# Kernel optimization log

Hardware: AMD Instinct MI355X
Metric: run time of the kernel (lower is better)

## Reference

```python
import jax, jax.numpy as jnp
import numpy as np

B, S, DIN, DH, DOUT = 8, 2048, 512, 1024, 16


def setup_inputs() -> dict:
    key = jax.random.key(0)
    ks = jax.random.split(key, 7)
    x = jax.random.normal(ks[0], (B, S, DIN), dtype=jnp.float32)
    # MLP params (Linear stores W as [in, out] here; we apply x @ W + b)
    w1 = jax.random.normal(ks[1], (DIN, DH), dtype=jnp.float32) / np.sqrt(DIN)
    b1 = jnp.zeros((DH,), dtype=jnp.float32)
    w2 = jax.random.normal(ks[2], (DH, DH), dtype=jnp.float32) / np.sqrt(DH)
    b2 = jnp.zeros((DH,), dtype=jnp.float32)
    w3 = jax.random.normal(ks[3], (DH, DOUT), dtype=jnp.float32) / np.sqrt(DH)
    b3 = jnp.zeros((DOUT,), dtype=jnp.float32)
    # decay buffer: exact dyadics 1 - 2^-(c+3), matches init_kwargs list
    decay = 1.0 - 2.0 ** (-(jnp.arange(DOUT, dtype=jnp.float32) + 3.0))
    # D[i, t, c] = decay_c^(t - i) for t >= i else 0 (upper triangular per channel)
    idx = jnp.arange(S)
    exps = idx[None, :] - idx[:, None]            # [S, S], t - i
    mask = (exps >= 0).astype(jnp.float32)        # triu mask
    exps_c = jnp.maximum(exps, 0).astype(jnp.float32)
    D = mask[:, :, None] * (decay[None, None, :] ** exps_c[:, :, None])  # [S, S, DOUT]
    return {"input_temporal": x, "w1": w1, "b1": b1, "w2": w2, "b2": b2,
            "w3": w3, "b3": b3, "D": D}


def reference(input_temporal, w1, b1, w2, b2, w3, b3, D):
    # 3-layer MLP (dropout=0 -> identity in eval)
    h = jax.nn.relu(input_temporal @ w1 + b1)
    h = jax.nn.relu(h @ w2 + b2)
    o = h @ w3 + b3                               # [B, S, DOUT]
    # decay-weighted causal mixing: out[b,t,c] = sum_{i<=t} o[b,i,c] * decay_c^(t-i)
    # (equivalent to torch repeat+multiply+sum, without materializing [B,S,S,D])
    mixed = jnp.einsum('bic,itc->btc', o, D)
    # extra running cumsum as in the original forward
    return jnp.cumsum(mixed, axis=1)
```

## Files before the change

kernel.cpp:

```cpp
#include <hip/hip_runtime.h>

typedef unsigned int u32;
typedef unsigned short u16;
typedef float f32x4 __attribute__((ext_vector_type(4)));
typedef short bf16x8 __attribute__((ext_vector_type(8)));

__device__ __forceinline__ u16 f2bf(float f) {
  u32 u = __builtin_bit_cast(u32, f);
  u += 0x7FFFu + ((u >> 16) & 1u);
  return (u16)(u >> 16);
}
__device__ __forceinline__ void gload_lds16(const void* g, void* l) {
  __builtin_amdgcn_global_load_lds(
      (const __attribute__((address_space(1))) void*)g,
      (__attribute__((address_space(3))) void*)l, 16, 0, 0);
}

__global__ __launch_bounds__(256) void cast_f32_bf16_k(
    const float4* __restrict__ in, uint2* __restrict__ out, int n4) {
  int i = blockIdx.x * 256 + threadIdx.x;
  if (i < n4) {
    float4 v = in[i];
    uint2 o;
    o.x = (u32)f2bf(v.x) | ((u32)f2bf(v.y) << 16);
    o.y = (u32)f2bf(v.z) | ((u32)f2bf(v.w) << 16);
    out[i] = o;
  }
}

__global__ __launch_bounds__(256) void transpose3_k(
    const float* __restrict__ w1, u16* __restrict__ w1t,
    const float* __restrict__ w2, u16* __restrict__ w2t,
    const float* __restrict__ w3, u16* __restrict__ w3t) {
  __shared__ float tile[32][33];
  const float* in; u16* out; int R, C;
  if (blockIdx.z == 0)      { in = w1; out = w1t; R = 512;  C = 1024; }
  else if (blockIdx.z == 1) { in = w2; out = w2t; R = 1024; C = 1024; }
  else                      { in = w3; out = w3t; R = 1024; C = 16;   }
  int c0 = blockIdx.x * 32, r0 = blockIdx.y * 32;
  if (c0 >= C || r0 >= R) return;
  int tx = threadIdx.x, ty = threadIdx.y;
  #pragma unroll
  for (int j = 0; j < 4; j++) {
    int r = r0 + ty + j * 8, c = c0 + tx;
    if (r < R && c < C) tile[ty + j * 8][tx] = in[(size_t)r * C + c];
  }
  __syncthreads();
  #pragma unroll
  for (int j = 0; j < 4; j++) {
    int c = c0 + ty + j * 8, r = r0 + tx;
    if (r < R && c < C) out[(size_t)c * R + r] = f2bf(tile[tx][ty + j * 8]);
  }
}

__global__ __launch_bounds__(512, 2) void gemm_bt_k(
    const u16* __restrict__ A, const u16* __restrict__ Bt,
    const float* __restrict__ bias, u16* __restrict__ C,
    int M, int N, int K) {
  __shared__ __align__(16) char lds[3 * 49152];
  const int tid = threadIdx.x;
  const int rr = blockIdx.x;
  const int xcd = rr & 7, slot_id = rr >> 3;
  const int bm = (xcd << 3) | (slot_id >> 3);
  const int bn = slot_id & 7;
  const int wave = tid >> 6, lane = tid & 63;
  const int wm = wave >> 1, wn = wave & 1;
  const int l15 = lane & 15, l4 = lane >> 4;
  const int NT = K >> 6;
  const size_t arow0 = (size_t)bm * 256, brow0 = (size_t)bn * 128;

  f32x4 acc[4][4];
  #pragma unroll
  for (int m = 0; m < 4; m++)
    #pragma unroll
    for (int n = 0; n < 4; n++) acc[m][n] = (f32x4){0.f, 0.f, 0.f, 0.f};

  auto stage = [&](int kt, int s) {
    char* sA = lds + s * 49152;
    char* sB = sA + 32768;
    #pragma unroll
    for (int j = 0; j < 4; j++) {
      int ch = tid + j * 512;
      int row = ch >> 3;
      int col8 = (ch & 7) ^ (row & 7);
      gload_lds16(A + (arow0 + row) * K + kt * 64 + col8 * 8, sA + ch * 16);
    }
    #pragma unroll
    for (int j = 0; j < 2; j++) {
      int ch = tid + j * 512;
      int row = ch >> 3;
      int col8 = (ch & 7) ^ (row & 7);
      gload_lds16(Bt + (brow0 + row) * K + kt * 64 + col8 * 8, sB + ch * 16);
    }
  };

  stage(0, 0);
  stage(1, 1);
  asm volatile("s_waitcnt vmcnt(6)" ::: "memory");
  __builtin_amdgcn_s_barrier();

  for (int t = 0; t < NT; t++) {
    const int s = t % 3;
    const char* sA = lds + s * 49152;
    const char* sB = sA + 32768;

    bf16x8 bfr[2][4];
    #pragma unroll
    for (int ks = 0; ks < 2; ks++)
      #pragma unroll
      for (int n = 0; n < 4; n++) {
        int r = wn * 64 + n * 16 + l15;
        bfr[ks][n] = *(const bf16x8*)(sB + r * 128 +
                                      (((ks * 4 + l4) ^ (r & 7)) << 4));
      }
    bf16x8 af0[2][2];
    #pragma unroll
    for (int m = 0; m < 2; m++)
      #pragma unroll
      for (int ks = 0; ks < 2; ks++) {
        int r = wm * 64 + m * 16 + l15;
        af0[m][ks] = *(const bf16x8*)(sA + r * 128 +
                                      (((ks * 4 + l4) ^ (r & 7)) << 4));
      }
    if (t + 2 < NT) stage(t + 2, (t + 2) % 3);

    __builtin_amdgcn_s_barrier();
    asm volatile("s_waitcnt lgkmcnt(0)" ::: "memory");
    __builtin_amdgcn_sched_barrier(0);
    __builtin_amdgcn_s_setprio(1);
    #pragma unroll
    for (int m = 0; m < 2; m++)
      #pragma unroll
      for (int n = 0; n < 4; n++)
        #pragma unroll
        for (int ks = 0; ks < 2; ks++)
          acc[m][n] = __builtin_amdgcn_mfma_f32_16x16x32_bf16(
              af0[m][ks], bfr[ks][n], acc[m][n], 0, 0, 0);
    __builtin_amdgcn_s_setprio(0);

    bf16x8 af1[2][2];
    #pragma unroll
    for (int m = 0; m < 2; m++)
      #pragma unroll
      for (int ks = 0; ks < 2; ks++) {
        int r = wm * 64 + (m + 2) * 16 + l15;
        af1[m][ks] = *(const bf16x8*)(sA + r * 128 +
                                      (((ks * 4 + l4) ^ (r & 7)) << 4));
      }
    __builtin_amdgcn_s_barrier();
    asm volatile("s_waitcnt lgkmcnt(0)" ::: "memory");
    __builtin_amdgcn_sched_barrier(0);
    __builtin_amdgcn_s_setprio(1);
    #pragma unroll
    for (int m = 0; m < 2; m++)
      #pragma unroll
      for (int n = 0; n < 4; n++)
        #pragma unroll
        for (int ks = 0; ks < 2; ks++)
          acc[m + 2][n] = __builtin_amdgcn_mfma_f32_16x16x32_bf16(
              af1[m][ks], bfr[ks][n], acc[m + 2][n], 0, 0, 0);
    __builtin_amdgcn_s_setprio(0);

    if (t + 1 < NT) {
      if (t + 2 < NT)
        asm volatile("s_waitcnt vmcnt(6)" ::: "memory");
      else
        asm volatile("s_waitcnt vmcnt(0)" ::: "memory");
      __builtin_amdgcn_s_barrier();
    }
  }

  #pragma unroll
  for (int n = 0; n < 4; n++) {
    int col = bn * 128 + wn * 64 + n * 16 + l15;
    float bv = bias[col];
    #pragma unroll
    for (int m = 0; m < 4; m++) {
      int row0 = bm * 256 + wm * 64 + m * 16 + l4 * 4;
      #pragma unroll
      for (int r = 0; r < 4; r++) {
        float v = acc[m][n][r] + bv;
        v = v > 0.f ? v : 0.f;
        C[(size_t)(row0 + r) * N + col] = f2bf(v);
      }
    }
  }
}

__global__ __launch_bounds__(512, 2) void gemm2f_k(
    const u16* __restrict__ A, const u16* __restrict__ Bt,
    const float* __restrict__ bias, const u16* __restrict__ w3t,
    float* __restrict__ part, int M, int N, int K) {
  __shared__ __align__(16) char lds[131072];
  const int tid = threadIdx.x;
  const int rr = blockIdx.x;
  const int xcd = rr & 7, slot_id = rr >> 3;
  const int bm = (xcd << 3) | (slot_id >> 2);
  const int bn = slot_id & 3;
  const int wave = tid >> 6, lane = tid & 63;
  const int wm = wave >> 2, wn = wave & 3;
  const int l15 = lane & 15, l4 = lane >> 4;
  const int NT = K >> 5;
  const size_t arow0 = (size_t)bm * 256, brow0 = (size_t)bn * 256;

  f32x4 acc[4][8];
  #pragma unroll
  for (int p = 0; p < 4; p++)
    #pragma unroll
    for (int q = 0; q < 8; q++) acc[p][q] = (f32x4){0.f, 0.f, 0.f, 0.f};

  auto stage = [&](int kt, int s) {
    char* sA = lds + s * 32768;
    char* sB = sA + 16384;
    #pragma unroll
    for (int j = 0; j < 2; j++) {
      int ch = tid + j * 512;
      int row = ch >> 2;
      int col4 = (ch & 3) ^ (row & 3);
      gload_lds16(A + (arow0 + row) * K + kt * 32 + col4 * 8, sA + ch * 16);
    }
    #pragma unroll
    for (int j = 0; j < 2; j++) {
      int ch = tid + j * 512;
      int row = ch >> 2;
      int col4 = (ch & 3) ^ (row & 3);
      gload_lds16(Bt + (brow0 + row) * K + kt * 32 + col4 * 8, sB + ch * 16);
    }
  };

  stage(0, 0);
  stage(1, 1);
  asm volatile("s_waitcnt vmcnt(4)" ::: "memory");
  __builtin_amdgcn_s_barrier();

  for (int t = 0; t < NT; t++) {
    const int s = t % 3;
    const char* sA = lds + s * 32768;
    const char* sB = sA + 16384;

    bf16x8 bfr[4];
    #pragma unroll
    for (int n = 0; n < 4; n++) {
      int r = wn * 64 + n * 16 + l15;
      bfr[n] = *(const bf16x8*)(sB + r * 64 + ((l4 ^ (r & 3)) << 4));
    }
    bf16x8 af0[4];
    #pragma unroll
    for (int m = 0; m < 4; m++) {
      int r = wm * 128 + m * 16 + l15;
      af0[m] = *(const bf16x8*)(sA + r * 64 + ((l4 ^ (r & 3)) << 4));
    }
    if (t + 2 < NT) stage(t + 2, (t + 2) % 3);

    __builtin_amdgcn_s_barrier();
    asm volatile("s_waitcnt lgkmcnt(0)" ::: "memory");
    __builtin_amdgcn_sched_barrier(0);
    __builtin_amdgcn_s_setprio(1);
    #pragma unroll
    for (int p = 0; p < 4; p++)
      #pragma unroll
      for (int q = 0; q < 4; q++)
        acc[p][q] = __builtin_amdgcn_mfma_f32_16x16x32_bf16(
            bfr[p], af0[q], acc[p][q], 0, 0, 0);
    __builtin_amdgcn_s_setprio(0);

    bf16x8 af1[4];
    #pragma unroll
    for (int m = 0; m < 4; m++) {
      int r = wm * 128 + (m + 4) * 16 + l15;
      af1[m] = *(const bf16x8*)(sA + r * 64 + ((l4 ^ (r & 3)) << 4));
    }
    __builtin_amdgcn_s_barrier();
    asm volatile("s_waitcnt lgkmcnt(0)" ::: "memory");
    __builtin_amdgcn_sched_barrier(0);
    __builtin_amdgcn_s_setprio(1);
    #pragma unroll
    for (int p = 0; p < 4; p++)
      #pragma unroll
      for (int q = 0; q < 4; q++)
        acc[p][q + 4] = __builtin_amdgcn_mfma_f32_16x16x32_bf16(
            bfr[p], af1[q], acc[p][q + 4], 0, 0, 0);
    __builtin_amdgcn_s_setprio(0);

    if (t + 1 < NT) {
      if (t + 2 < NT)
        asm volatile("s_waitcnt vmcnt(4)" ::: "memory");
      else
        asm volatile("s_waitcnt vmcnt(0)" ::: "memory");
      __builtin_amdgcn_s_barrier();
    }
  }

  __builtin_amdgcn_s_barrier();
  #pragma unroll
  for (int p = 0; p < 4; p++) {
    float4 bv = *(const float4*)(bias + wn * 64 + p * 16 + l4 * 4);
    int colb = (wn * 64 + p * 16 + l4 * 4) * 2;
    #pragma unroll
    for (int q = 0; q < 8; q++) {
      int hrow = wm * 128 + q * 16 + l15;
      float v0 = acc[p][q][0] + bv.x; v0 = v0 > 0.f ? v0 : 0.f;
      float v1 = acc[p][q][1] + bv.y; v1 = v1 > 0.f ? v1 : 0.f;
      float v2 = acc[p][q][2] + bv.z; v2 = v2 > 0.f ? v2 : 0.f;
      float v3 = acc[p][q][3] + bv.w; v3 = v3 > 0.f ? v3 : 0.f;
      uint2 pk;
      pk.x = (u32)f2bf(v0) | ((u32)f2bf(v1) << 16);
      pk.y = (u32)f2bf(v2) | ((u32)f2bf(v3) << 16);
      *(uint2*)(lds + hrow * 512 + (colb ^ ((hrow & 7) << 4))) = pk;
    }
  }
  __builtin_amdgcn_s_barrier();

  bf16x8 wf[8];
  {
    const u16* w3row = w3t + (size_t)l15 * 1024 + bn * 256 + l4 * 8;
    #pragma unroll
    for (int kk = 0; kk < 8; kk++)
      wf[kk] = *(const bf16x8*)(w3row + kk * 32);
  }
  #pragma unroll
  for (int g = 0; g < 2; g++) {
    int row0 = wave * 32 + g * 16;
    int row = row0 + l15;
    f32x4 oacc = (f32x4){0.f, 0.f, 0.f, 0.f};
    #pragma unroll
    for (int kk = 0; kk < 8; kk++) {
      bf16x8 hf = *(const bf16x8*)(lds + row * 512 +
                                   ((kk * 64 + l4 * 16) ^ ((row & 7) << 4)));
      oacc = __builtin_amdgcn_mfma_f32_16x16x32_bf16(hf, wf[kk], oacc,
                                                     0, 0, 0);
    }
    int grow = bm * 256 + row0 + l4 * 4;
    int b = grow >> 11, s = grow & 2047;
    float4 st = {oacc[0], oacc[1], oacc[2], oacc[3]};
    *(float4*)(part + ((size_t)bn * 128 + b * 16 + l15) * 2048 + s) = st;
  }
}

__global__ __launch_bounds__(64) void scan_k(
    const float* __restrict__ part, const float* __restrict__ b3,
    float* __restrict__ out) {
  const int chain = blockIdx.x;
  const int lane = threadIdx.x;
  const int b = chain >> 4, c = chain & 15;
  const float dinv = __builtin_bit_cast(float, (u32)((127 - (c + 3)) << 23));
  const float d = 1.f - dinv;
  const float b3c = b3[c];

  float o[32];
  #pragma unroll
  for (int i = 0; i < 8; i++) {
    float4 acc4 = {b3c, b3c, b3c, b3c};
    #pragma unroll
    for (int p = 0; p < 4; p++) {
      const float4* src = (const float4*)(part + (size_t)p * 262144 +
                                          (size_t)chain * 2048 + lane * 32);
      float4 v = src[i];
      acc4.x += v.x; acc4.y += v.y; acc4.z += v.z; acc4.w += v.w;
    }
    o[i * 4 + 0] = acc4.x; o[i * 4 + 1] = acc4.y;
    o[i * 4 + 2] = acc4.z; o[i * 4 + 3] = acc4.w;
  }

  float M = 0.f, A = 0.f, P = 1.f, S = 0.f;
  #pragma unroll
  for (int i = 0; i < 32; i++) {
    M = d * M + o[i];
    A += M;
    P *= d;
    S = d * S + d;
  }

  #pragma unroll
  for (int off = 1; off < 64; off <<= 1) {
    float Pp = __shfl_up(P, off, 64);
    float Mp = __shfl_up(M, off, 64);
    float Sp = __shfl_up(S, off, 64);
    float Ap = __shfl_up(A, off, 64);
    if (lane >= off) {
      float A2 = Ap + S * Mp + A;
      float S2 = Sp + S * Pp;
      float M2 = P * Mp + M;
      float P2 = Pp * P;
      A = A2; S = S2; M = M2; P = P2;
    }
  }
  float m0 = __shfl_up(M, 1, 64);
  float a0 = __shfl_up(A, 1, 64);
  if (lane == 0) { m0 = 0.f; a0 = 0.f; }

  float* dst = out + (size_t)b * 32768 + (size_t)(lane * 32) * 16 + c;
  float m = m0, a = a0;
  #pragma unroll
  for (int i = 0; i < 32; i++) {
    m = d * m + o[i];
    a += m;
    dst[i * 16] = a;
  }
}

extern "C" void kernel_launch(void* const* d_in, const int* in_sizes, int n_in,
                              void* d_out, int out_size, void* d_ws, size_t ws_size,
                              hipStream_t stream) {
  const float* x  = (const float*)d_in[0];
  const float* w1 = (const float*)d_in[1];
  const float* b1 = (const float*)d_in[2];
  const float* w2 = (const float*)d_in[3];
  const float* b2 = (const float*)d_in[4];
  const float* w3 = (const float*)d_in[5];
  const float* b3 = (const float*)d_in[6];
  float* out = (float*)d_out;

  char* ws = (char*)d_ws;
  size_t off = 0;
  u16* A1   = (u16*)(ws + off); off += (size_t)16384 * 512 * 2;
  u16* h1   = (u16*)(ws + off); off += (size_t)16384 * 1024 * 2;
  u16* w1t  = (u16*)(ws + off); off += (size_t)1024 * 512 * 2;
  u16* w2t  = (u16*)(ws + off); off += (size_t)1024 * 1024 * 2;
  u16* w3t  = (u16*)(ws + off); off += (size_t)16 * 1024 * 2;
  float* part = (float*)(ws + off); off += (size_t)4 * 128 * 2048 * 4;

  cast_f32_bf16_k<<<8192, 256, 0, stream>>>((const float4*)x, (uint2*)A1,
                                            16384 * 512 / 4);
  transpose3_k<<<dim3(32, 32, 3), dim3(32, 8), 0, stream>>>(
      w1, w1t, w2, w2t, w3, w3t);

  gemm_bt_k<<<512, 512, 0, stream>>>(A1, w1t, b1, h1, 16384, 1024, 512);
  gemm2f_k<<<256, 512, 0, stream>>>(h1, w2t, b2, w3t, part,
                                    16384, 1024, 1024);
  scan_k<<<128, 64, 0, stream>>>(part, b3, out);
}
```

Measured before the change: 85.97 us.

## Fuse fp32-to-bf16 input cast into first GEMM via LDS conversion

Removes the separate cast kernel and the bf16 copy of the input. The first GEMM now stages fp32 input tiles straight into LDS with a K tile of 32, converts them to bf16 with v_cvt_pk_bf16_f32 while loading fragments, and swaps the MFMA operand order so the epilogue can write packed 4-wide bf16 stores with a vector bias load. This saves one full read and write pass over the input and one launch. In exchange it doubles the number of K iterations and barriers per tile, and each A tile now moves twice the bytes into LDS.

```diff
diff --git a/kernel.cpp b/kernel.cpp
--- a/kernel.cpp
+++ b/kernel.cpp
@@ -15,17 +15,10 @@
       (const __attribute__((address_space(1))) void*)g,
       (__attribute__((address_space(3))) void*)l, 16, 0, 0);
 }
-
-__global__ __launch_bounds__(256) void cast_f32_bf16_k(
-    const float4* __restrict__ in, uint2* __restrict__ out, int n4) {
-  int i = blockIdx.x * 256 + threadIdx.x;
-  if (i < n4) {
-    float4 v = in[i];
-    uint2 o;
-    o.x = (u32)f2bf(v.x) | ((u32)f2bf(v.y) << 16);
-    o.y = (u32)f2bf(v.z) | ((u32)f2bf(v.w) << 16);
-    out[i] = o;
-  }
+__device__ __forceinline__ u32 cvtpk_bf16(float lo, float hi) {
+  u32 r;
+  asm("v_cvt_pk_bf16_f32 %0, %1, %2" : "=v"(r) : "v"(lo), "v"(hi));
+  return r;
 }
 
 __global__ __launch_bounds__(256) void transpose3_k(
@@ -53,11 +46,11 @@
   }
 }
 
-__global__ __launch_bounds__(512, 2) void gemm_bt_k(
-    const u16* __restrict__ A, const u16* __restrict__ Bt,
+__global__ __launch_bounds__(512, 2) void gemm1f_k(
+    const float* __restrict__ X, const u16* __restrict__ Bt,
     const float* __restrict__ bias, u16* __restrict__ C,
     int M, int N, int K) {
-  __shared__ __align__(16) char lds[3 * 49152];
+  __shared__ __align__(16) char lds[3 * 40960];
   const int tid = threadIdx.x;
   const int rr = blockIdx.x;
   const int xcd = rr & 7, slot_id = rr >> 3;
@@ -66,62 +59,64 @@
   const int wave = tid >> 6, lane = tid & 63;
   const int wm = wave >> 1, wn = wave & 1;
   const int l15 = lane & 15, l4 = lane >> 4;
-  const int NT = K >> 6;
+  const int NT = K >> 5;
   const size_t arow0 = (size_t)bm * 256, brow0 = (size_t)bn * 128;
 
   f32x4 acc[4][4];
   #pragma unroll
-  for (int m = 0; m < 4; m++)
-    #pragma unroll
-    for (int n = 0; n < 4; n++) acc[m][n] = (f32x4){0.f, 0.f, 0.f, 0.f};
+  for (int n = 0; n < 4; n++)
+    #pragma unroll
+    for (int m = 0; m < 4; m++) acc[n][m] = (f32x4){0.f, 0.f, 0.f, 0.f};
 
   auto stage = [&](int kt, int s) {
-    char* sA = lds + s * 49152;
+    char* sA = lds + s * 40960;
     char* sB = sA + 32768;
     #pragma unroll
     for (int j = 0; j < 4; j++) {
       int ch = tid + j * 512;
       int row = ch >> 3;
-      int col8 = (ch & 7) ^ (row & 7);
-      gload_lds16(A + (arow0 + row) * K + kt * 64 + col8 * 8, sA + ch * 16);
-    }
-    #pragma unroll
-    for (int j = 0; j < 2; j++) {
-      int ch = tid + j * 512;
-      int row = ch >> 3;
-      int col8 = (ch & 7) ^ (row & 7);
-      gload_lds16(Bt + (brow0 + row) * K + kt * 64 + col8 * 8, sB + ch * 16);
+      int g = (ch & 7) ^ (row & 7);
+      gload_lds16(X + (arow0 + row) * K + kt * 32 + g * 4, sA + ch * 16);
+    }
+    {
+      int ch = tid;
+      int row = ch >> 2;
+      int col4 = (ch & 3) ^ (row & 3);
+      gload_lds16(Bt + (brow0 + row) * K + kt * 32 + col4 * 8, sB + ch * 16);
     }
   };
 
   stage(0, 0);
   stage(1, 1);
-  asm volatile("s_waitcnt vmcnt(6)" ::: "memory");
+  asm volatile("s_waitcnt vmcnt(5)" ::: "memory");
   __builtin_amdgcn_s_barrier();
 
   for (int t = 0; t < NT; t++) {
     const int s = t % 3;
-    const char* sA = lds + s * 49152;
+    const char* sA = lds + s * 40960;
     const char* sB = sA + 32768;
 
-    bf16x8 bfr[2][4];
-    #pragma unroll
-    for (int ks = 0; ks < 2; ks++)
-      #pragma unroll
-      for (int n = 0; n < 4; n++) {
-        int r = wn * 64 + n * 16 + l15;
-        bfr[ks][n] = *(const bf16x8*)(sB + r * 128 +
-                                      (((ks * 4 + l4) ^ (r & 7)) << 4));
-      }
-    bf16x8 af0[2][2];
-    #pragma unroll
-    for (int m = 0; m < 2; m++)
-      #pragma unroll
-      for (int ks = 0; ks < 2; ks++) {
-        int r = wm * 64 + m * 16 + l15;
-        af0[m][ks] = *(const bf16x8*)(sA + r * 128 +
-                                      (((ks * 4 + l4) ^ (r & 7)) << 4));
-      }
+    bf16x8 bfr[4];
+    #pragma unroll
+    for (int n = 0; n < 4; n++) {
+      int r = wn * 64 + n * 16 + l15;
+      bfr[n] = *(const bf16x8*)(sB + r * 64 + ((l4 ^ (r & 3)) << 4));
+    }
+    bf16x8 af[4];
+    #pragma unroll
+    for (int m = 0; m < 4; m++) {
+      int r = wm * 64 + m * 16 + l15;
+      int g0 = ((l4 * 2 + 0) ^ (r & 7)) << 4;
+      int g1 = ((l4 * 2 + 1) ^ (r & 7)) << 4;
+      f32x4 a0 = *(const f32x4*)(sA + r * 128 + g0);
+      f32x4 a1 = *(const f32x4*)(sA + r * 128 + g1);
+      u32 p0 = cvtpk_bf16(a0[0], a0[1]);
+      u32 p1 = cvtpk_bf16(a0[2], a0[3]);
+      u32 p2 = cvtpk_bf16(a1[0], a1[1]);
+      u32 p3 = cvtpk_bf16(a1[2], a1[3]);
+      uint4 packed = {p0, p1, p2, p3};
+      af[m] = __builtin_bit_cast(bf16x8, packed);
+    }
     if (t + 2 < NT) stage(t + 2, (t + 2) % 3);
 
     __builtin_amdgcn_s_barrier();
@@ -129,41 +124,16 @@
     __builtin_amdgcn_sched_barrier(0);
     __builtin_amdgcn_s_setprio(1);
     #pragma unroll
-    for (int m = 0; m < 2; m++)
+    for (int n = 0; n < 4; n++)
       #pragma unroll
-      for (int n = 0; n < 4; n++)
-        #pragma unroll
-        for (int ks = 0; ks < 2; ks++)
-          acc[m][n] = __builtin_amdgcn_mfma_f32_16x16x32_bf16(
-              af0[m][ks], bfr[ks][n], acc[m][n], 0, 0, 0);
-    __builtin_amdgcn_s_setprio(0);
-
-    bf16x8 af1[2][2];
-    #pragma unroll
-    for (int m = 0; m < 2; m++)
-      #pragma unroll
-      for (int ks = 0; ks < 2; ks++) {
-        int r = wm * 64 + (m + 2) * 16 + l15;
-        af1[m][ks] = *(const bf16x8*)(sA + r * 128 +
-                                      (((ks * 4 + l4) ^ (r & 7)) << 4));
-      }
-    __builtin_amdgcn_s_barrier();
-    asm volatile("s_waitcnt lgkmcnt(0)" ::: "memory");
-    __builtin_amdgcn_sched_barrier(0);
-    __builtin_amdgcn_s_setprio(1);
-    #pragma unroll
-    for (int m = 0; m < 2; m++)
-      #pragma unroll
-      for (int n = 0; n < 4; n++)
-        #pragma unroll
-        for (int ks = 0; ks < 2; ks++)
-          acc[m + 2][n] = __builtin_amdgcn_mfma_f32_16x16x32_bf16(
-              af1[m][ks], bfr[ks][n], acc[m + 2][n], 0, 0, 0);
+      for (int m = 0; m < 4; m++)
+        acc[n][m] = __builtin_amdgcn_mfma_f32_16x16x32_bf16(
+            bfr[n], af[m], acc[n][m], 0, 0, 0);
     __builtin_amdgcn_s_setprio(0);
 
     if (t + 1 < NT) {
       if (t + 2 < NT)
-        asm volatile("s_waitcnt vmcnt(6)" ::: "memory");
+        asm volatile("s_waitcnt vmcnt(5)" ::: "memory");
       else
         asm volatile("s_waitcnt vmcnt(0)" ::: "memory");
       __builtin_amdgcn_s_barrier();
@@ -172,17 +142,19 @@
 
   #pragma unroll
   for (int n = 0; n < 4; n++) {
-    int col = bn * 128 + wn * 64 + n * 16 + l15;
-    float bv = bias[col];
+    int col0 = bn * 128 + wn * 64 + n * 16 + l4 * 4;
+    float4 bv = *(const float4*)(bias + col0);
     #pragma unroll
     for (int m = 0; m < 4; m++) {
-      int row0 = bm * 256 + wm * 64 + m * 16 + l4 * 4;
-      #pragma unroll
-      for (int r = 0; r < 4; r++) {
-        float v = acc[m][n][r] + bv;
-        v = v > 0.f ? v : 0.f;
-        C[(size_t)(row0 + r) * N + col] = f2bf(v);
-      }
+      int row = bm * 256 + wm * 64 + m * 16 + l15;
+      float v0 = acc[n][m][0] + bv.x; v0 = v0 > 0.f ? v0 : 0.f;
+      float v1 = acc[n][m][1] + bv.y; v1 = v1 > 0.f ? v1 : 0.f;
+      float v2 = acc[n][m][2] + bv.z; v2 = v2 > 0.f ? v2 : 0.f;
+      float v3 = acc[n][m][3] + bv.w; v3 = v3 > 0.f ? v3 : 0.f;
+      uint2 pk;
+      pk.x = (u32)f2bf(v0) | ((u32)f2bf(v1) << 16);
+      pk.y = (u32)f2bf(v2) | ((u32)f2bf(v3) << 16);
+      *(uint2*)(C + (size_t)row * N + col0) = pk;
     }
   }
 }
@@ -413,19 +385,16 @@
 
   char* ws = (char*)d_ws;
   size_t off = 0;
-  u16* A1   = (u16*)(ws + off); off += (size_t)16384 * 512 * 2;
   u16* h1   = (u16*)(ws + off); off += (size_t)16384 * 1024 * 2;
   u16* w1t  = (u16*)(ws + off); off += (size_t)1024 * 512 * 2;
   u16* w2t  = (u16*)(ws + off); off += (size_t)1024 * 1024 * 2;
   u16* w3t  = (u16*)(ws + off); off += (size_t)16 * 1024 * 2;
   float* part = (float*)(ws + off); off += (size_t)4 * 128 * 2048 * 4;
 
-  cast_f32_bf16_k<<<8192, 256, 0, stream>>>((const float4*)x, (uint2*)A1,
-                                            16384 * 512 / 4);
   transpose3_k<<<dim3(32, 32, 3), dim3(32, 8), 0, stream>>>(
       w1, w1t, w2, w2t, w3, w3t);
 
-  gemm_bt_k<<<512, 512, 0, stream>>>(A1, w1t, b1, h1, 16384, 1024, 512);
+  gemm1f_k<<<512, 512, 0, stream>>>(x, w1t, b1, h1, 16384, 1024, 512);
   gemm2f_k<<<256, 512, 0, stream>>>(h1, w2t, b2, w3t, part,
                                     16384, 1024, 1024);
   scan_k<<<128, 64, 0, stream>>>(part, b3, out);
```

After: 93.16 us. 1.08x slower.

## Merge cast and transpose launches; make GEMM1 blocks compute two N tiles

Applied to the files above, without the earlier changes.

The input cast and weight transpose kernels are merged into one launch, with the block index split between the transpose work and the cast work. The first GEMM now launches 256 blocks, and each block loops over two adjacent 128-wide N tiles with the same A rows. The aim is to cut one kernel launch and have one persistent wave of blocks instead of two, improving A reuse through cache. The cost is less parallelism per launch and a serial two-pass loop per block, with A re-staged from global memory on each pass.

```diff
diff --git a/kernel.cpp b/kernel.cpp
--- a/kernel.cpp
+++ b/kernel.cpp
@@ -16,30 +16,32 @@
       (__attribute__((address_space(3))) void*)l, 16, 0, 0);
 }
 
-__global__ __launch_bounds__(256) void cast_f32_bf16_k(
-    const float4* __restrict__ in, uint2* __restrict__ out, int n4) {
-  int i = blockIdx.x * 256 + threadIdx.x;
-  if (i < n4) {
-    float4 v = in[i];
+__global__ __launch_bounds__(256) void prep_k(
+    const float* __restrict__ x, uint2* __restrict__ A1,
+    const float* __restrict__ w1, u16* __restrict__ w1t,
+    const float* __restrict__ w2, u16* __restrict__ w2t,
+    const float* __restrict__ w3, u16* __restrict__ w3t) {
+  const int bid = blockIdx.x;
+  const int tid = threadIdx.x;
+  if (bid >= 3072) {
+    int i = (bid - 3072) * 256 + tid;
+    float4 v = ((const float4*)x)[i];
     uint2 o;
     o.x = (u32)f2bf(v.x) | ((u32)f2bf(v.y) << 16);
     o.y = (u32)f2bf(v.z) | ((u32)f2bf(v.w) << 16);
-    out[i] = o;
-  }
-}
-
-__global__ __launch_bounds__(256) void transpose3_k(
-    const float* __restrict__ w1, u16* __restrict__ w1t,
-    const float* __restrict__ w2, u16* __restrict__ w2t,
-    const float* __restrict__ w3, u16* __restrict__ w3t) {
+    A1[i] = o;
+    return;
+  }
   __shared__ float tile[32][33];
+  const int z = bid >> 10, t = bid & 1023;
+  const int bx = t & 31, by = t >> 5;
   const float* in; u16* out; int R, C;
-  if (blockIdx.z == 0)      { in = w1; out = w1t; R = 512;  C = 1024; }
-  else if (blockIdx.z == 1) { in = w2; out = w2t; R = 1024; C = 1024; }
-  else                      { in = w3; out = w3t; R = 1024; C = 16;   }
-  int c0 = blockIdx.x * 32, r0 = blockIdx.y * 32;
+  if (z == 0)      { in = w1; out = w1t; R = 512;  C = 1024; }
+  else if (z == 1) { in = w2; out = w2t; R = 1024; C = 1024; }
+  else             { in = w3; out = w3t; R = 1024; C = 16;   }
+  int c0 = bx * 32, r0 = by * 32;
   if (c0 >= C || r0 >= R) return;
-  int tx = threadIdx.x, ty = threadIdx.y;
+  int tx = tid & 31, ty = tid >> 5;
   #pragma unroll
   for (int j = 0; j < 4; j++) {
     int r = r0 + ty + j * 8, c = c0 + tx;
@@ -53,135 +55,142 @@
   }
 }
 
-__global__ __launch_bounds__(512, 2) void gemm_bt_k(
+__global__ __launch_bounds__(512, 2) void gemm1p_k(
     const u16* __restrict__ A, const u16* __restrict__ Bt,
     const float* __restrict__ bias, u16* __restrict__ C,
     int M, int N, int K) {
   __shared__ __align__(16) char lds[3 * 49152];
   const int tid = threadIdx.x;
   const int rr = blockIdx.x;
-  const int xcd = rr & 7, slot_id = rr >> 3;
-  const int bm = (xcd << 3) | (slot_id >> 3);
-  const int bn = slot_id & 7;
+  const int xcd = rr & 7, s_id = rr >> 3;
+  const int bm = (xcd << 3) | (s_id >> 2);
+  const int bnBase = (s_id & 3) << 1;
   const int wave = tid >> 6, lane = tid & 63;
   const int wm = wave >> 1, wn = wave & 1;
   const int l15 = lane & 15, l4 = lane >> 4;
   const int NT = K >> 6;
-  const size_t arow0 = (size_t)bm * 256, brow0 = (size_t)bn * 128;
-
-  f32x4 acc[4][4];
-  #pragma unroll
-  for (int m = 0; m < 4; m++)
-    #pragma unroll
-    for (int n = 0; n < 4; n++) acc[m][n] = (f32x4){0.f, 0.f, 0.f, 0.f};
-
-  auto stage = [&](int kt, int s) {
-    char* sA = lds + s * 49152;
-    char* sB = sA + 32768;
-    #pragma unroll
-    for (int j = 0; j < 4; j++) {
-      int ch = tid + j * 512;
-      int row = ch >> 3;
-      int col8 = (ch & 7) ^ (row & 7);
-      gload_lds16(A + (arow0 + row) * K + kt * 64 + col8 * 8, sA + ch * 16);
-    }
-    #pragma unroll
-    for (int j = 0; j < 2; j++) {
-      int ch = tid + j * 512;
-      int row = ch >> 3;
-      int col8 = (ch & 7) ^ (row & 7);
-      gload_lds16(Bt + (brow0 + row) * K + kt * 64 + col8 * 8, sB + ch * 16);
-    }
-  };
-
-  stage(0, 0);
-  stage(1, 1);
-  asm volatile("s_waitcnt vmcnt(6)" ::: "memory");
-  __builtin_amdgcn_s_barrier();
-
-  for (int t = 0; t < NT; t++) {
-    const int s = t % 3;
-    const char* sA = lds + s * 49152;
-    const char* sB = sA + 32768;
-
-    bf16x8 bfr[2][4];
-    #pragma unroll
-    for (int ks = 0; ks < 2; ks++)
-      #pragma unroll
-      for (int n = 0; n < 4; n++) {
-        int r = wn * 64 + n * 16 + l15;
-        bfr[ks][n] = *(const bf16x8*)(sB + r * 128 +
-                                      (((ks * 4 + l4) ^ (r & 7)) << 4));
+  const size_t arow0 = (size_t)bm * 256;
+
+  for (int p = 0; p < 2; p++) {
+    const int bn = bnBase + p;
+    const size_t brow0 = (size_t)bn * 128;
+
+    f32x4 acc[4][4];
+    #pragma unroll
+    for (int m = 0; m < 4; m++)
+      #pragma unroll
+      for (int n = 0; n < 4; n++) acc[m][n] = (f32x4){0.f, 0.f, 0.f, 0.f};
+
+    auto stage = [&](int kt, int s) {
+      char* sA = lds + s * 49152;
+      char* sB = sA + 32768;
+      #pragma unroll
+      for (int j = 0; j < 4; j++) {
+        int ch = tid + j * 512;
+        int row = ch >> 3;
+        int col8 = (ch & 7) ^ (row & 7);
+        gload_lds16(A + (arow0 + row) * K + kt * 64 + col8 * 8, sA + ch * 16);
       }
-    bf16x8 af0[2][2];
-    #pragma unroll
-    for (int m = 0; m < 2; m++)
-      #pragma unroll
-      for (int ks = 0; ks < 2; ks++) {
-        int r = wm * 64 + m * 16 + l15;
-        af0[m][ks] = *(const bf16x8*)(sA + r * 128 +
-                                      (((ks * 4 + l4) ^ (r & 7)) << 4));
+      #pragma unroll
+      for (int j = 0; j < 2; j++) {
+        int ch = tid + j * 512;
+        int row = ch >> 3;
+        int col8 = (ch & 7) ^ (row & 7);
+        gload_lds16(Bt + (brow0 + row) * K + kt * 64 + col8 * 8, sB + ch * 16);
       }
-    if (t + 2 < NT) stage(t + 2, (t + 2) % 3);
-
+    };
+
+    if (p) __builtin_amdgcn_s_barrier();
+
+    stage(0, 0);
+    stage(1, 1);
+    asm volatile("s_waitcnt vmcnt(6)" ::: "memory");
     __builtin_amdgcn_s_barrier();
-    asm volatile("s_waitcnt lgkmcnt(0)" ::: "memory");
-    __builtin_amdgcn_sched_barrier(0);
-    __builtin_amdgcn_s_setprio(1);
-    #pragma unroll
-    for (int m = 0; m < 2; m++)
-      #pragma unroll
-      for (int n = 0; n < 4; n++)
-        #pragma unroll
-        for (int ks = 0; ks < 2; ks++)
-          acc[m][n] = __builtin_amdgcn_mfma_f32_16x16x32_bf16(
-              af0[m][ks], bfr[ks][n], acc[m][n], 0, 0, 0);
-    __builtin_amdgcn_s_setprio(0);
-
-    bf16x8 af1[2][2];
-    #pragma unroll
-    for (int m = 0; m < 2; m++)
-      #pragma unroll
-      for (int ks = 0; ks < 2; ks++) {
-        int r = wm * 64 + (m + 2) * 16 + l15;
-        af1[m][ks] = *(const bf16x8*)(sA + r * 128 +
-                                      (((ks * 4 + l4) ^ (r & 7)) << 4));
+
+    for (int t = 0; t < NT; t++) {
+      const int s = t % 3;
+      const char* sA = lds + s * 49152;
+      const char* sB = sA + 32768;
+
+      bf16x8 bfr[2][4];
+      #pragma unroll
+      for (int ks = 0; ks < 2; ks++)
+        #pragma unroll
+        for (int n = 0; n < 4; n++) {
+          int r = wn * 64 + n * 16 + l15;
+          bfr[ks][n] = *(const bf16x8*)(sB + r * 128 +
+                                        (((ks * 4 + l4) ^ (r & 7)) << 4));
+        }
+      bf16x8 af0[2][2];
+      #pragma unroll
+      for (int m = 0; m < 2; m++)
+        #pragma unroll
+        for (int ks = 0; ks < 2; ks++) {
+          int r = wm * 64 + m * 16 + l15;
+          af0[m][ks] = *(const bf16x8*)(sA + r * 128 +
+                                        (((ks * 4 + l4) ^ (r & 7)) << 4));
+        }
+      if (t + 2 < NT) stage(t + 2, (t + 2) % 3);
+
+      __builtin_amdgcn_s_barrier();
+      asm volatile("s_waitcnt lgkmcnt(0)" ::: "memory");
+      __builtin_amdgcn_sched_barrier(0);
+      __builtin_amdgcn_s_setprio(1);
+      #pragma unroll
+      for (int m = 0; m < 2; m++)
+        #pragma unroll
+        for (int n = 0; n < 4; n++)
+          #pragma unroll
+          for (int ks = 0; ks < 2; ks++)
+            acc[m][n] = __builtin_amdgcn_mfma_f32_16x16x32_bf16(
+                af0[m][ks], bfr[ks][n], acc[m][n], 0, 0, 0);
+      __builtin_amdgcn_s_setprio(0);
+
+      bf16x8 af1[2][2];
+      #pragma unroll
+      for (int m = 0; m < 2; m++)
+        #pragma unroll
+        for (int ks = 0; ks < 2; ks++) {
+          int r = wm * 64 + (m + 2) * 16 + l15;
+          af1[m][ks] = *(const bf16x8*)(sA + r * 128 +
+                                        (((ks * 4 + l4) ^ (r & 7)) << 4));
+        }
+      __builtin_amdgcn_s_barrier();
+      asm volatile("s_waitcnt lgkmcnt(0)" ::: "memory");
+      __builtin_amdgcn_sched_barrier(0);
+      __builtin_amdgcn_s_setprio(1);
+      #pragma unroll
+      for (int m = 0; m < 2; m++)
+        #pragma unroll
+        for (int n = 0; n < 4; n++)
+          #pragma unroll
+          for (int ks = 0; ks < 2; ks++)
+            acc[m + 2][n] = __builtin_amdgcn_mfma_f32_16x16x32_bf16(
+                af1[m][ks], bfr[ks][n], acc[m + 2][n], 0, 0, 0);
+      __builtin_amdgcn_s_setprio(0);
+
+      if (t + 1 < NT) {
+        if (t + 2 < NT)
+          asm volatile("s_waitcnt vmcnt(6)" ::: "memory");
+        else
+          asm volatile("s_waitcnt vmcnt(0)" ::: "memory");
+        __builtin_amdgcn_s_barrier();
       }
-    __builtin_amdgcn_s_barrier();
-    asm volatile("s_waitcnt lgkmcnt(0)" ::: "memory");
-    __builtin_amdgcn_sched_barrier(0);
-    __builtin_amdgcn_s_setprio(1);
-    #pragma unroll
-    for (int m = 0; m < 2; m++)
-      #pragma unroll
-      for (int n = 0; n < 4; n++)
-        #pragma unroll
-        for (int ks = 0; ks < 2; ks++)
-          acc[m + 2][n] = __builtin_amdgcn_mfma_f32_16x16x32_bf16(
-              af1[m][ks], bfr[ks][n], acc[m + 2][n], 0, 0, 0);
-    __builtin_amdgcn_s_setprio(0);
-
-    if (t + 1 < NT) {
-      if (t + 2 < NT)
-        asm volatile("s_waitcnt vmcnt(6)" ::: "memory");
-      else
-        asm volatile("s_waitcnt vmcnt(0)" ::: "memory");
-      __builtin_amdgcn_s_barrier();
-    }
-  }
-
-  #pragma unroll
-  for (int n = 0; n < 4; n++) {
-    int col = bn * 128 + wn * 64 + n * 16 + l15;
-    float bv = bias[col];
-    #pragma unroll
-    for (int m = 0; m < 4; m++) {
-      int row0 = bm * 256 + wm * 64 + m * 16 + l4 * 4;
-      #pragma unroll
-      for (int r = 0; r < 4; r++) {
-        float v = acc[m][n][r] + bv;
-        v = v > 0.f ? v : 0.f;
-        C[(size_t)(row0 + r) * N + col] = f2bf(v);
+    }
+
+    #pragma unroll
+    for (int n = 0; n < 4; n++) {
+      int col = bn * 128 + wn * 64 + n * 16 + l15;
+      float bv = bias[col];
+      #pragma unroll
+      for (int m = 0; m < 4; m++) {
+        int row0 = bm * 256 + wm * 64 + m * 16 + l4 * 4;
+        #pragma unroll
+        for (int r = 0; r < 4; r++) {
+          float v = acc[m][n][r] + bv;
+          v = v > 0.f ? v : 0.f;
+          C[(size_t)(row0 + r) * N + col] = f2bf(v);
+        }
       }
     }
   }
@@ -420,12 +429,8 @@
   u16* w3t  = (u16*)(ws + off); off += (size_t)16 * 1024 * 2;
   float* part = (float*)(ws + off); off += (size_t)4 * 128 * 2048 * 4;
 
-  cast_f32_bf16_k<<<8192, 256, 0, stream>>>((const float4*)x, (uint2*)A1,
-                                            16384 * 512 / 4);
-  transpose3_k<<<dim3(32, 32, 3), dim3(32, 8), 0, stream>>>(
-      w1, w1t, w2, w2t, w3, w3t);
-
-  gemm_bt_k<<<512, 512, 0, stream>>>(A1, w1t, b1, h1, 16384, 1024, 512);
+  prep_k<<<11264, 256, 0, stream>>>(x, (uint2*)A1, w1, w1t, w2, w2t, w3, w3t);
+  gemm1p_k<<<256, 512, 0, stream>>>(A1, w1t, b1, h1, 16384, 1024, 512);
   gemm2f_k<<<256, 512, 0, stream>>>(h1, w2t, b2, w3t, part,
                                     16384, 1024, 1024);
   scan_k<<<128, 64, 0, stream>>>(part, b3, out);
```

After: 84.20 us. -2.1%, faster.
